# Performance work log

Measured on AMD Instinct MI355X. Metric: run time of the kernel, lower is better.

Reference implementation:

```python
import jax, jax.numpy as jnp
import numpy as np

N = 10000   # nodes
E = 50000   # edges
G = 8       # graphs in batch
IN = 16     # input_dim
H = 64      # hidden_dim
EH = 32     # edge-network hidden
L = 3       # num ECC layers
BN_EPS = 1e-5


def _xavier(k, shape):
    fan_in, fan_out = shape[-2], shape[-1]
    s = jnp.sqrt(2.0 / (fan_in + fan_out)).astype(jnp.float32)
    return jax.random.normal(k, shape, jnp.float32) * s


def setup_inputs() -> dict:
    key = jax.random.key(0)
    ks = jax.random.split(key, 10)
    x = jax.random.normal(ks[0], (N, IN), jnp.float32)
    edge_index = jax.random.randint(ks[1], (2, E), 0, N, jnp.int32)
    batch = jnp.sort(jax.random.randint(ks[2], (N,), 0, G, jnp.int32))
    return {
        "x": x,
        "edge_index": edge_index,
        "batch": batch,
        "emb_w": _xavier(ks[3], (IN, H)),
        "emb_b": jnp.zeros((H,), jnp.float32),
        "e1_w": _xavier(ks[4], (L, 1, EH)),
        "e1_b": jnp.zeros((L, EH), jnp.float32),
        "e2_w": _xavier(ks[5], (L, EH, H * H)),
        "e2_b": jnp.zeros((L, H * H), jnp.float32),
        "self_w": _xavier(ks[6], (L, H, H)),
        "self_b": jnp.zeros((L, H), jnp.float32),
        "bn_g": jnp.ones((L, H), jnp.float32),
        "bn_b": jnp.zeros((L, H), jnp.float32),
        "cls_w": _xavier(ks[7], (2 * H, 1)),
        "cls_b": jnp.zeros((1,), jnp.float32),
    }


def reference(x, edge_index, batch, emb_w, emb_b, e1_w, e1_b, e2_w, e2_b,
              self_w, self_b, bn_g, bn_b, cls_w, cls_b):
    src, dst = edge_index[0], edge_index[1]
    # in-degree of targets for 'mean' aggregation (computed once; edge structure fixed)
    deg = jnp.clip(jax.ops.segment_sum(jnp.ones((E,), x.dtype), dst, num_segments=N), 1.0, None)

    h = x @ emb_w + emb_b  # [N, H] input embedding
    for l in range(L):
        # edge_attr: L2 distance between first 3 hidden channels of endpoints, [E,1]
        d = h[src, :3] - h[dst, :3]
        ea = jnp.sqrt(jnp.sum(d * d, axis=1, keepdims=True))
        # edge network -> per-edge dynamic weight matrix [E, H, H]
        hid = jax.nn.relu(ea @ e1_w[l] + e1_b[l])          # [E, EH]
        W = (hid @ e2_w[l] + e2_b[l]).reshape(E, H, H)
        # message: x_j (source features) times per-edge weight
        msg = jnp.einsum('ei,eio->eo', h[src], W)          # [E, H]
        agg = jax.ops.segment_sum(msg, dst, num_segments=N) / deg[:, None]
        h2 = agg + h @ self_w[l] + self_b[l]               # ECC output + self transform
        # BatchNorm1d (training-mode batch stats, biased variance), then ReLU
        mu = h2.mean(axis=0)
        var = h2.var(axis=0)
        h = jax.nn.relu(bn_g[l] * (h2 - mu) * jax.lax.rsqrt(var + BN_EPS) + bn_b[l])
        # dropout is a no-op in eval mode

    cnt = jnp.clip(jax.ops.segment_sum(jnp.ones((N,), h.dtype), batch, num_segments=G), 1.0, None)
    h_mean = jax.ops.segment_sum(h, batch, num_segments=G) / cnt[:, None]
    h_max = jax.ops.segment_max(h, batch, num_segments=G)
    h_pooled = jnp.concatenate([h_mean, h_max], axis=1)    # [G, 2H]
    return jax.nn.sigmoid(h_pooled @ cls_w + cls_b)        # [G, 1]
```

## Files before the change

kernel.cpp:

```cpp
#include <hip/hip_runtime.h>
#include <math.h>

#define N_NODES 10000
#define N_EDGES 50000
#define N_GRAPHS 8
#define IN_DIM  16
#define HID     64
#define EHID    32
#define NLAYER  3
#define NK      33
#define BN_EPS  1e-5f
#define POOL_BLOCKS 63
#define LAYER_BLOCKS 625
#define MAXDEG  64

#define FB_EMBED 2500
#define FB_S2    (16 * NK * NLAYER)
#define FB_AUX   3
#define FB_TOTAL (FB_EMBED + FB_S2 + FB_AUX)

#define OFF_H0     0u
#define OFF_H2A    640000u
#define OFF_H2B    1280000u
#define OFF_ATAB   1920000u
#define OFF_CTAB   2325504u
#define OFF_S      2731008u
#define OFF_NB     2731136u
#define OFF_CUR    2731200u
#define OFF_CSRC   2741200u
#define OFF_STATS  3381200u
#define OFF_GSUM   3381584u
#define OFF_GMAX   3382096u
#define OFF_GCNT   3382608u
#define OFF_CNTR   3382616u

__device__ __forceinline__ float rl(float v, int i) {
    return __int_as_float(__builtin_amdgcn_readlane(__float_as_int(v), i));
}

__device__ __forceinline__ void bn_coef(const float* __restrict__ sPrev,
                                        const float* __restrict__ gPrev,
                                        const float* __restrict__ bPrev,
                                        int c, float& sc, float& sf) {
    float mu  = sPrev[c] * (1.0f / N_NODES);
    float var = fmaf(-mu, mu, sPrev[64 + c] * (1.0f / N_NODES));
    float rstd = 1.0f / sqrtf(var + BN_EPS);
    sc = gPrev[c] * rstd;
    sf = fmaf(-sc, mu, bPrev[c]);
}

__device__ __forceinline__ int bp_list(const float* __restrict__ e1w,
                                       const float* __restrict__ e1b,
                                       int l, float* t) {
    int c = 0;
    for (int j = 0; j < EHID; ++j) {
        float a = e1w[l * EHID + j], b = e1b[l * EHID + j];
        if ((a > 0.f && b < 0.f) || (a < 0.f && b > 0.f)) t[c++] = -b / a;
    }
    for (int i = 1; i < c; ++i) {
        float v = t[i]; int j = i - 1;
        while (j >= 0 && t[j] > v) { t[j + 1] = t[j]; --j; }
        t[j + 1] = v;
    }
    return c;
}

__global__ void k_front(const float* __restrict__ x, const float* __restrict__ emb_w,
                        const float* __restrict__ emb_b,
                        const float* __restrict__ e1w, const float* __restrict__ e1b,
                        const float* __restrict__ e2w, const float* __restrict__ e2b,
                        float* __restrict__ s_arr, int* __restrict__ nb,
                        int* __restrict__ cur, float* __restrict__ stats,
                        float* __restrict__ gsum, float* __restrict__ gmax,
                        int* __restrict__ gcnt, int* __restrict__ counter,
                        float* __restrict__ Atab, float* __restrict__ Ctab,
                        float* __restrict__ h0) {
    int b = blockIdx.x, tid = threadIdx.x;
    if (b < FB_EMBED) {
        int idx = b * 256 + tid;
        int n = idx >> 6, o = idx & 63;
        const float* xr = x + n * IN_DIM;
        float acc = emb_b[o];
        #pragma unroll
        for (int i = 0; i < IN_DIM; ++i) acc = fmaf(xr[i], emb_w[i * HID + o], acc);
        h0[idx] = acc;
    } else if (b < FB_EMBED + FB_S2) {
        __shared__ float st[EHID];
        __shared__ int snb;
        __shared__ float sma[EHID], smb[EHID];
        __shared__ float4 rA[4][64], rC[4][64];
        int job = b - FB_EMBED;
        int qq  = job / (NK * NLAYER);
        int rem = job % (NK * NLAYER);
        int k = rem / NLAYER, l = rem % NLAYER;
        if (tid == 0) {
            float t[EHID];
            int c = bp_list(e1w, e1b, l, t);
            snb = c;
            for (int i = 0; i < c; ++i) st[i] = t[i];
        }
        __syncthreads();
        int nbl = snb;
        if (k > nbl) return;
        if (tid < EHID) {
            float a = e1w[l * EHID + tid], bb = e1b[l * EHID + tid];
            float lo = (k == 0) ? 0.f : st[k - 1];
            float hi = st[k];
            float p  = (k == nbl) ? (lo + 1.0f) : 0.5f * (lo + hi);
            float m  = (p * a + bb > 0.f) ? 1.f : 0.f;
            sma[tid] = m * a;
            smb[tid] = m * bb;
        }
        __syncthreads();
        int lane6 = tid & 63, grp = tid >> 6;
        int f4 = qq * 64 + lane6;
        const float4* w4 = (const float4*)e2w;
        float4 accA = make_float4(0.f, 0.f, 0.f, 0.f);
        float4 accC = make_float4(0.f, 0.f, 0.f, 0.f);
        #pragma unroll
        for (int jj = 0; jj < 8; ++jj) {
            int j = grp * 8 + jj;
            float4 w = w4[(l * EHID + j) * 1024 + f4];
            float ma = sma[j], mb = smb[j];
            accA.x = fmaf(ma, w.x, accA.x); accA.y = fmaf(ma, w.y, accA.y);
            accA.z = fmaf(ma, w.z, accA.z); accA.w = fmaf(ma, w.w, accA.w);
            accC.x = fmaf(mb, w.x, accC.x); accC.y = fmaf(mb, w.y, accC.y);
            accC.z = fmaf(mb, w.z, accC.z); accC.w = fmaf(mb, w.w, accC.w);
        }
        rA[grp][lane6] = accA;
        rC[grp][lane6] = accC;
        __syncthreads();
        if (grp == 0) {
            float4 a0 = rA[0][lane6], a1 = rA[1][lane6], a2 = rA[2][lane6], a3 = rA[3][lane6];
            float4 c0 = rC[0][lane6], c1 = rC[1][lane6], c2 = rC[2][lane6], c3 = rC[3][lane6];
            float4 eb = ((const float4*)(e2b + l * HID * HID))[f4];
            float4 A, C;
            A.x = a0.x + a1.x + a2.x + a3.x; A.y = a0.y + a1.y + a2.y + a3.y;
            A.z = a0.z + a1.z + a2.z + a3.z; A.w = a0.w + a1.w + a2.w + a3.w;
            C.x = c0.x + c1.x + c2.x + c3.x + eb.x; C.y = c0.y + c1.y + c2.y + c3.y + eb.y;
            C.z = c0.z + c1.z + c2.z + c3.z + eb.z; C.w = c0.w + c1.w + c2.w + c3.w + eb.w;
            ((float4*)(Atab + (l * NK + k) * (HID * HID)))[f4] = A;
            ((float4*)(Ctab + (l * NK + k) * (HID * HID)))[f4] = C;
        }
    } else {
        int a = b - FB_EMBED - FB_S2;
        if (a == 0) {
            for (int i = tid; i < N_NODES; i += 256) cur[i] = 0;
        } else if (a == 1) {
            for (int i = tid; i < N_GRAPHS * HID; i += 256) { gsum[i] = 0.f; gmax[i] = 0.f; }
            if (tid < N_GRAPHS) gcnt[tid] = 0;
            if (tid == 0) *counter = 0;
        } else {
            for (int i = tid; i < NLAYER * 128; i += 256) stats[i] = 0.f;
            if (tid < NLAYER) {
                float t[EHID];
                int c = bp_list(e1w, e1b, tid, t);
                nb[tid] = c;
                for (int i = 0; i < c; ++i) s_arr[tid * NK + i] = t[i];
            }
        }
    }
}

__global__ void k_fill(const int* __restrict__ ei, int* __restrict__ cur,
                       int* __restrict__ csrc) {
    int e = blockIdx.x * blockDim.x + threadIdx.x;
    if (e < N_EDGES) {
        int dst = ei[N_EDGES + e];
        int pos = atomicAdd(&cur[dst], 1);
        if (pos < MAXDEG) csrc[dst * MAXDEG + pos] = ei[e];
    }
}

__global__ void __launch_bounds__(256, 3)
k_layer(const float* __restrict__ hb, int useBN,
        const float* __restrict__ sPrev, const float* __restrict__ gPrev,
        const float* __restrict__ bPrev,
        const int* __restrict__ csrc, const int* __restrict__ deg,
        const float* __restrict__ Atab, const float* __restrict__ Ctab,
        const float* __restrict__ s_arr, const int* __restrict__ nbp, int l,
        const float* __restrict__ sw_l, const float* __restrict__ sb_l,
        float* __restrict__ h2out, float* __restrict__ statsOut) {
    __shared__ float smW[3 * HID * HID];
    __shared__ float sRed[2][4][HID];
    int tid = threadIdx.x, wid = tid >> 6, lane = tid & 63;
    int nb = nbp[l];
    const float* A0 = Atab + l * NK * HID * HID;
    const float* C0 = Ctab + l * NK * HID * HID;
    {
        float4* s4 = (float4*)smW;
        const float4* w4 = (const float4*)sw_l;
        const float4* a4 = (const float4*)A0;
        const float4* c4 = (const float4*)C0;
        #pragma unroll
        for (int p = 0; p < 4; ++p) {
            int j = p * 256 + tid;
            s4[j] = w4[j];
            s4[1024 + j] = a4[j];
            s4[2048 + j] = c4[j];
        }
    }
    __syncthreads();
    float sc = 0.f, sf = 0.f;
    if (useBN) bn_coef(sPrev, gPrev, bPrev, lane, sc, sf);
    float sbv = sb_l[lane];
    int nodeBase = blockIdx.x * 16 + wid * 4;

    float hvv[4];
    int cnts[4]; int maxc = 0;
    #pragma unroll
    for (int c = 0; c < 4; ++c) {
        float hv = hb[(nodeBase + c) * HID + lane];
        if (useBN) hv = fmaxf(fmaf(sc, hv, sf), 0.f);
        hvv[c] = hv;
        int cc = min(deg[nodeBase + c], MAXDEG);
        cnts[c] = cc;
        maxc = max(maxc, cc);
    }

    float pp[4] = {0.f, 0.f, 0.f, 0.f};
    float qq[4] = {0.f, 0.f, 0.f, 0.f};
    float aggE[4] = {0.f, 0.f, 0.f, 0.f};

    if (nb == 0) {
        for (int j0 = 0; j0 < maxc; j0 += 4) {
            float g[4][4];
            #pragma unroll
            for (int c = 0; c < 4; ++c) {
                int rem = cnts[c] - j0;
                if (rem > 0) {
                    const int* cp = &csrc[(nodeBase + c) * MAXDEG + j0];
                    g[c][0] = hb[cp[0] * HID + lane];
                    if (rem > 1) g[c][1] = hb[cp[1] * HID + lane];
                    if (rem > 2) g[c][2] = hb[cp[2] * HID + lane];
                    if (rem > 3) g[c][3] = hb[cp[3] * HID + lane];
                }
            }
            #pragma unroll
            for (int c = 0; c < 4; ++c) {
                int rem = cnts[c] - j0;
                #pragma unroll
                for (int u = 0; u < 4; ++u) {
                    if (u < rem) {
                        float hs = g[c][u];
                        if (useBN) hs = fmaxf(fmaf(sc, hs, sf), 0.f);
                        float diff = hs - hvv[c];
                        float d0 = rl(diff, 0), d1 = rl(diff, 1), d2 = rl(diff, 2);
                        float ea = sqrtf(fmaf(d0, d0, fmaf(d1, d1, d2 * d2)));
                        pp[c] = fmaf(ea, hs, pp[c]);
                        qq[c] += hs;
                    }
                }
            }
        }
    } else {
        #pragma unroll
        for (int c = 0; c < 4; ++c) {
            float hv = hvv[c];
            float aggv = 0.f;
            const int base = (nodeBase + c) * MAXDEG;
            for (int j = 0; j < cnts[c]; ++j) {
                int src = csrc[base + j];
                float hs = hb[src * HID + lane];
                if (useBN) hs = fmaxf(fmaf(sc, hs, sf), 0.f);
                float diff = hs - hv;
                float d0 = rl(diff, 0), d1 = rl(diff, 1), d2 = rl(diff, 2);
                float ea = sqrtf(fmaf(d0, d0, fmaf(d1, d1, d2 * d2)));
                int k = 0;
                for (int i = 0; i < nb; ++i) k += (ea > s_arr[l * NK + i]) ? 1 : 0;
                const float* A = Atab + (l * NK + k) * (HID * HID);
                const float* C = Ctab + (l * NK + k) * (HID * HID);
                float au = 0.f, cu = 0.f;
                for (int i = 0; i < HID; ++i) {
                    float hi = rl(hs, i);
                    au = fmaf(hi, A[i * HID + lane], au);
                    cu = fmaf(hi, C[i * HID + lane], cu);
                }
                aggv += fmaf(ea, au, cu);
            }
            aggE[c] = aggv;
        }
    }

    float acc[4], agg[4];
    #pragma unroll
    for (int c = 0; c < 4; ++c) { acc[c] = sbv; agg[c] = 0.f; }
    #pragma unroll
    for (int i = 0; i < HID; ++i) {
        float ws = smW[i * HID + lane];
        float wa = smW[HID * HID + i * HID + lane];
        float wc = smW[2 * HID * HID + i * HID + lane];
        #pragma unroll
        for (int c = 0; c < 4; ++c) {
            acc[c] = fmaf(rl(hvv[c], i), ws, acc[c]);
            agg[c] = fmaf(rl(pp[c], i), wa, agg[c]);
            agg[c] = fmaf(rl(qq[c], i), wc, agg[c]);
        }
    }

    float ls = 0.f, ls2 = 0.f;
    #pragma unroll
    for (int c = 0; c < 4; ++c) {
        int node = nodeBase + c;
        float invd = 1.0f / fmaxf((float)deg[node], 1.0f);
        float v = fmaf(agg[c] + aggE[c], invd, acc[c]);
        h2out[node * HID + lane] = v;
        ls += v; ls2 = fmaf(v, v, ls2);
    }
    sRed[0][wid][lane] = ls;
    sRed[1][wid][lane] = ls2;
    __syncthreads();
    if (tid < HID) {
        float s  = sRed[0][0][tid] + sRed[0][1][tid] + sRed[0][2][tid] + sRed[0][3][tid];
        float s2 = sRed[1][0][tid] + sRed[1][1][tid] + sRed[1][2][tid] + sRed[1][3][tid];
        atomicAdd(&statsOut[tid], s);
        atomicAdd(&statsOut[64 + tid], s2);
    }
}

__global__ void k_bnpool(const float* __restrict__ h2cur, const float* __restrict__ s2,
                         const float* __restrict__ g2, const float* __restrict__ b2,
                         const int* __restrict__ batch,
                         float* __restrict__ gsum, float* __restrict__ gmax,
                         int* __restrict__ gcnt, int* __restrict__ counter,
                         const float* __restrict__ cw, const float* __restrict__ cb,
                         float* __restrict__ out) {
    int tid = threadIdx.x;
    int wid = (blockIdx.x * 256 + tid) >> 6, lane = tid & 63;
    float sc, sf; bn_coef(s2, g2, b2, lane, sc, sf);
    int n0 = wid * 40;
    int n1 = min(n0 + 40, N_NODES);
    float asum = 0.f, amax = 0.f;
    int cb2 = -1, run = 0;
    for (int n = n0; n < n1; ++n) {
        int b = batch[n];
        float v = fmaxf(fmaf(sc, h2cur[n * HID + lane], sf), 0.f);
        if (b != cb2) {
            if (cb2 >= 0) {
                atomicAdd(&gsum[cb2 * HID + lane], asum);
                atomicMax((int*)&gmax[cb2 * HID + lane], __float_as_int(amax));
                if (lane == 0) atomicAdd(&gcnt[cb2], run);
            }
            cb2 = b; asum = v; amax = v; run = 1;
        } else {
            asum += v; amax = fmaxf(amax, v); ++run;
        }
    }
    if (cb2 >= 0) {
        atomicAdd(&gsum[cb2 * HID + lane], asum);
        atomicMax((int*)&gmax[cb2 * HID + lane], __float_as_int(amax));
        if (lane == 0) atomicAdd(&gcnt[cb2], run);
    }
    __threadfence();
    __shared__ int lastFlag;
    if (tid == 0) {
        int old = __hip_atomic_fetch_add(counter, 1, __ATOMIC_ACQ_REL, __HIP_MEMORY_SCOPE_AGENT);
        lastFlag = (old == POOL_BLOCKS - 1);
    }
    __syncthreads();
    if (lastFlag && tid < N_GRAPHS) {
        int g = tid;
        float cnt = fmaxf((float)__hip_atomic_load(&gcnt[g], __ATOMIC_RELAXED, __HIP_MEMORY_SCOPE_AGENT), 1.f);
        float acc = cb[0];
        for (int o2 = 0; o2 < HID; ++o2) {
            float sv = __hip_atomic_load(&gsum[g * HID + o2], __ATOMIC_RELAXED, __HIP_MEMORY_SCOPE_AGENT);
            acc = fmaf(sv / cnt, cw[o2], acc);
        }
        for (int o2 = 0; o2 < HID; ++o2) {
            int iv = __hip_atomic_load((int*)&gmax[g * HID + o2], __ATOMIC_RELAXED, __HIP_MEMORY_SCOPE_AGENT);
            acc = fmaf(__int_as_float(iv), cw[HID + o2], acc);
        }
        out[g] = 1.0f / (1.0f + expf(-acc));
    }
}

extern "C" void kernel_launch(void* const* d_in, const int* in_sizes, int n_in,
                              void* d_out, int out_size, void* d_ws, size_t ws_size,
                              hipStream_t stream) {
    const float* x      = (const float*)d_in[0];
    const int*   ei     = (const int*)  d_in[1];
    const int*   batch  = (const int*)  d_in[2];
    const float* emb_w  = (const float*)d_in[3];
    const float* emb_b  = (const float*)d_in[4];
    const float* e1_w   = (const float*)d_in[5];
    const float* e1_b   = (const float*)d_in[6];
    const float* e2_w   = (const float*)d_in[7];
    const float* e2_b   = (const float*)d_in[8];
    const float* self_w = (const float*)d_in[9];
    const float* self_b = (const float*)d_in[10];
    const float* bn_g   = (const float*)d_in[11];
    const float* bn_b   = (const float*)d_in[12];
    const float* cls_w  = (const float*)d_in[13];
    const float* cls_b  = (const float*)d_in[14];
    float* outp = (float*)d_out;

    float* wsf = (float*)d_ws;
    float* h0     = wsf + OFF_H0;
    float* h2a    = wsf + OFF_H2A;
    float* h2b    = wsf + OFF_H2B;
    float* Atab   = wsf + OFF_ATAB;
    float* Ctab   = wsf + OFF_CTAB;
    float* s_arr  = wsf + OFF_S;
    int*   nb     = (int*)(wsf + OFF_NB);
    int*   cur    = (int*)(wsf + OFF_CUR);
    int*   csrc   = (int*)(wsf + OFF_CSRC);
    float* stats  = wsf + OFF_STATS;
    float* gsum   = wsf + OFF_GSUM;
    float* gmax   = wsf + OFF_GMAX;
    int*   gcnt   = (int*)(wsf + OFF_GCNT);
    int*   cntr   = (int*)(wsf + OFF_CNTR);

    k_front<<<FB_TOTAL, 256, 0, stream>>>(x, emb_w, emb_b, e1_w, e1_b, e2_w, e2_b,
                                          s_arr, nb, cur, stats, gsum, gmax, gcnt, cntr,
                                          Atab, Ctab, h0);
    k_fill<<<(N_EDGES + 255) / 256, 256, 0, stream>>>(ei, cur, csrc);

    for (int l = 0; l < NLAYER; ++l) {
        const float* hb    = (l == 0) ? h0 : ((l == 1) ? h2a : h2b);
        float*       h2out = (l == 1) ? h2b : h2a;
        const float* sPrev = stats + (l - 1) * 128;
        const float* gPrev = bn_g + (l - 1) * HID;
        const float* bPrev = bn_b + (l - 1) * HID;
        int useBN = (l > 0);
        k_layer<<<LAYER_BLOCKS, 256, 0, stream>>>(hb, useBN, sPrev, gPrev, bPrev,
                                                  csrc, cur,
                                                  Atab, Ctab, s_arr, nb, l,
                                                  self_w + l * HID * HID, self_b + l * HID,
                                                  h2out, stats + l * 128);
    }

    k_bnpool<<<POOL_BLOCKS, 256, 0, stream>>>(h2a, stats + 2 * 128, bn_g + 2 * HID, bn_b + 2 * HID,
                                              batch, gsum, gmax, gcnt, cntr, cls_w, cls_b, outp);
}
```

Before: 146.7 us.

## Fuse BN-pool-classifier tail into last layer kernel via grid-wide arrival counter

Removes the separate pooling kernel launch by having the last layer kernel count block arrivals on a global atomic. The first 63 blocks spin until all 625 blocks have finished, then apply the final BatchNorm/ReLU and graph pooling, and the last of them computes the classifier. This saves one kernel launch and its gap. It relies on the first 63 blocks staying resident while the remaining blocks get scheduled, and it adds spin-wait plus extra parameters and register pressure to the layer kernel.

```diff
diff --git a/kernel.cpp b/kernel.cpp
--- a/kernel.cpp
+++ b/kernel.cpp
@@ -33,6 +33,7 @@
 #define OFF_GMAX   3382096u
 #define OFF_GCNT   3382608u
 #define OFF_CNTR   3382616u
+#define OFF_ARR    3382620u
 
 __device__ __forceinline__ float rl(float v, int i) {
     return __int_as_float(__builtin_amdgcn_readlane(__float_as_int(v), i));
@@ -73,6 +74,7 @@
                         int* __restrict__ cur, float* __restrict__ stats,
                         float* __restrict__ gsum, float* __restrict__ gmax,
                         int* __restrict__ gcnt, int* __restrict__ counter,
+                        int* __restrict__ arr,
                         float* __restrict__ Atab, float* __restrict__ Ctab,
                         float* __restrict__ h0) {
     int b = blockIdx.x, tid = threadIdx.x;
@@ -149,7 +151,7 @@
         } else if (a == 1) {
             for (int i = tid; i < N_GRAPHS * HID; i += 256) { gsum[i] = 0.f; gmax[i] = 0.f; }
             if (tid < N_GRAPHS) gcnt[tid] = 0;
-            if (tid == 0) *counter = 0;
+            if (tid == 0) { *counter = 0; *arr = 0; }
         } else {
             for (int i = tid; i < NLAYER * 128; i += 256) stats[i] = 0.f;
             if (tid < NLAYER) {
@@ -180,7 +182,13 @@
         const float* __restrict__ Atab, const float* __restrict__ Ctab,
         const float* __restrict__ s_arr, const int* __restrict__ nbp, int l,
         const float* __restrict__ sw_l, const float* __restrict__ sb_l,
-        float* __restrict__ h2out, float* __restrict__ statsOut) {
+        float* __restrict__ h2out, float* __restrict__ statsOut,
+        int isLast, const int* __restrict__ batch,
+        const float* __restrict__ bn_g, const float* __restrict__ bn_b,
+        float* __restrict__ gsum, float* __restrict__ gmax,
+        int* __restrict__ gcnt, int* __restrict__ counter, int* __restrict__ arr,
+        const float* __restrict__ cls_w, const float* __restrict__ cls_b,
+        float* __restrict__ out) {
     __shared__ float smW[3 * HID * HID];
     __shared__ float sRed[2][4][HID];
     int tid = threadIdx.x, wid = tid >> 6, lane = tid & 63;
@@ -316,61 +324,69 @@
         atomicAdd(&statsOut[tid], s);
         atomicAdd(&statsOut[64 + tid], s2);
     }
-}
-
-__global__ void k_bnpool(const float* __restrict__ h2cur, const float* __restrict__ s2,
-                         const float* __restrict__ g2, const float* __restrict__ b2,
-                         const int* __restrict__ batch,
-                         float* __restrict__ gsum, float* __restrict__ gmax,
-                         int* __restrict__ gcnt, int* __restrict__ counter,
-                         const float* __restrict__ cw, const float* __restrict__ cb,
-                         float* __restrict__ out) {
-    int tid = threadIdx.x;
-    int wid = (blockIdx.x * 256 + tid) >> 6, lane = tid & 63;
-    float sc, sf; bn_coef(s2, g2, b2, lane, sc, sf);
-    int n0 = wid * 40;
-    int n1 = min(n0 + 40, N_NODES);
-    float asum = 0.f, amax = 0.f;
-    int cb2 = -1, run = 0;
-    for (int n = n0; n < n1; ++n) {
-        int b = batch[n];
-        float v = fmaxf(fmaf(sc, h2cur[n * HID + lane], sf), 0.f);
-        if (b != cb2) {
-            if (cb2 >= 0) {
-                atomicAdd(&gsum[cb2 * HID + lane], asum);
-                atomicMax((int*)&gmax[cb2 * HID + lane], __float_as_int(amax));
-                if (lane == 0) atomicAdd(&gcnt[cb2], run);
-            }
-            cb2 = b; asum = v; amax = v; run = 1;
-        } else {
-            asum += v; amax = fmaxf(amax, v); ++run;
-        }
-    }
-    if (cb2 >= 0) {
-        atomicAdd(&gsum[cb2 * HID + lane], asum);
-        atomicMax((int*)&gmax[cb2 * HID + lane], __float_as_int(amax));
-        if (lane == 0) atomicAdd(&gcnt[cb2], run);
-    }
-    __threadfence();
-    __shared__ int lastFlag;
+
+    if (!isLast) return;
+
+    __syncthreads();
     if (tid == 0) {
-        int old = __hip_atomic_fetch_add(counter, 1, __ATOMIC_ACQ_REL, __HIP_MEMORY_SCOPE_AGENT);
-        lastFlag = (old == POOL_BLOCKS - 1);
+        __threadfence();
+        __hip_atomic_fetch_add(arr, 1, __ATOMIC_ACQ_REL, __HIP_MEMORY_SCOPE_AGENT);
+    }
+    if (blockIdx.x >= POOL_BLOCKS) return;
+    if (tid == 0) {
+        while (__hip_atomic_load(arr, __ATOMIC_ACQUIRE, __HIP_MEMORY_SCOPE_AGENT) < LAYER_BLOCKS)
+            __builtin_amdgcn_s_sleep(2);
+        __threadfence();
     }
     __syncthreads();
-    if (lastFlag && tid < N_GRAPHS) {
-        int g = tid;
-        float cnt = fmaxf((float)__hip_atomic_load(&gcnt[g], __ATOMIC_RELAXED, __HIP_MEMORY_SCOPE_AGENT), 1.f);
-        float acc = cb[0];
-        for (int o2 = 0; o2 < HID; ++o2) {
-            float sv = __hip_atomic_load(&gsum[g * HID + o2], __ATOMIC_RELAXED, __HIP_MEMORY_SCOPE_AGENT);
-            acc = fmaf(sv / cnt, cw[o2], acc);
-        }
-        for (int o2 = 0; o2 < HID; ++o2) {
-            int iv = __hip_atomic_load((int*)&gmax[g * HID + o2], __ATOMIC_RELAXED, __HIP_MEMORY_SCOPE_AGENT);
-            acc = fmaf(__int_as_float(iv), cw[HID + o2], acc);
-        }
-        out[g] = 1.0f / (1.0f + expf(-acc));
+
+    {
+        float psc, psf; bn_coef(statsOut, bn_g + 2 * HID, bn_b + 2 * HID, lane, psc, psf);
+        int w = (blockIdx.x * 256 + tid) >> 6;
+        int n0 = w * 40;
+        int n1 = min(n0 + 40, N_NODES);
+        float asum = 0.f, amax = 0.f;
+        int cb2 = -1, run = 0;
+        for (int n = n0; n < n1; ++n) {
+            int b = batch[n];
+            float v = fmaxf(fmaf(psc, h2out[n * HID + lane], psf), 0.f);
+            if (b != cb2) {
+                if (cb2 >= 0) {
+                    atomicAdd(&gsum[cb2 * HID + lane], asum);
+                    atomicMax((int*)&gmax[cb2 * HID + lane], __float_as_int(amax));
+                    if (lane == 0) atomicAdd(&gcnt[cb2], run);
+                }
+                cb2 = b; asum = v; amax = v; run = 1;
+            } else {
+                asum += v; amax = fmaxf(amax, v); ++run;
+            }
+        }
+        if (cb2 >= 0) {
+            atomicAdd(&gsum[cb2 * HID + lane], asum);
+            atomicMax((int*)&gmax[cb2 * HID + lane], __float_as_int(amax));
+            if (lane == 0) atomicAdd(&gcnt[cb2], run);
+        }
+        __threadfence();
+        __shared__ int lastFlag;
+        if (tid == 0) {
+            int old = __hip_atomic_fetch_add(counter, 1, __ATOMIC_ACQ_REL, __HIP_MEMORY_SCOPE_AGENT);
+            lastFlag = (old == POOL_BLOCKS - 1);
+        }
+        __syncthreads();
+        if (lastFlag && tid < N_GRAPHS) {
+            int g = tid;
+            float cnt = fmaxf((float)__hip_atomic_load(&gcnt[g], __ATOMIC_RELAXED, __HIP_MEMORY_SCOPE_AGENT), 1.f);
+            float acc2 = cls_b[0];
+            for (int o2 = 0; o2 < HID; ++o2) {
+                float sv = __hip_atomic_load(&gsum[g * HID + o2], __ATOMIC_RELAXED, __HIP_MEMORY_SCOPE_AGENT);
+                acc2 = fmaf(sv / cnt, cls_w[o2], acc2);
+            }
+            for (int o2 = 0; o2 < HID; ++o2) {
+                int iv = __hip_atomic_load((int*)&gmax[g * HID + o2], __ATOMIC_RELAXED, __HIP_MEMORY_SCOPE_AGENT);
+                acc2 = fmaf(__int_as_float(iv), cls_w[HID + o2], acc2);
+            }
+            out[g] = 1.0f / (1.0f + expf(-acc2));
+        }
     }
 }
 
@@ -409,9 +425,10 @@
     float* gmax   = wsf + OFF_GMAX;
     int*   gcnt   = (int*)(wsf + OFF_GCNT);
     int*   cntr   = (int*)(wsf + OFF_CNTR);
+    int*   arr    = (int*)(wsf + OFF_ARR);
 
     k_front<<<FB_TOTAL, 256, 0, stream>>>(x, emb_w, emb_b, e1_w, e1_b, e2_w, e2_b,
-                                          s_arr, nb, cur, stats, gsum, gmax, gcnt, cntr,
+                                          s_arr, nb, cur, stats, gsum, gmax, gcnt, cntr, arr,
                                           Atab, Ctab, h0);
     k_fill<<<(N_EDGES + 255) / 256, 256, 0, stream>>>(ei, cur, csrc);
 
@@ -422,13 +439,14 @@
         const float* gPrev = bn_g + (l - 1) * HID;
         const float* bPrev = bn_b + (l - 1) * HID;
         int useBN = (l > 0);
+        int isLast = (l == NLAYER - 1);
         k_layer<<<LAYER_BLOCKS, 256, 0, stream>>>(hb, useBN, sPrev, gPrev, bPrev,
                                                   csrc, cur,
                                                   Atab, Ctab, s_arr, nb, l,
                                                   self_w + l * HID * HID, self_b + l * HID,
-                                                  h2out, stats + l * 128);
-    }
-
-    k_bnpool<<<POOL_BLOCKS, 256, 0, stream>>>(h2a, stats + 2 * 128, bn_g + 2 * HID, bn_b + 2 * HID,
-                                              batch, gsum, gmax, gcnt, cntr, cls_w, cls_b, outp);
-}
+                                                  h2out, stats + l * 128,
+                                                  isLast, batch, bn_g, bn_b,
+                                                  gsum, gmax, gcnt, cntr, arr,
+                                                  cls_w, cls_b, outp);
+    }
+}
```

After: 169.3 us. +15.4%, slower.
